# Kernel optimization log

Measured on AMD Instinct MI355X. Metric: run time of the kernel, lower is better.

The kernel has to match this reference:

```python
import jax, jax.numpy as jnp
import numpy as np

D_H = 2048      # d_hidden
D_E = 1408      # d_expert (per routed expert)
E = 8           # n_routed_experts
K = 2           # n_experts_per_token (top-k)
N_SHARED = 2    # n_shared_experts -> shared expert dim = D_E * N_SHARED
B, S = 1, 2048
D_S = D_E * N_SHARED


def setup_inputs() -> dict:
    key = jax.random.key(0)
    ks = jax.random.split(key, 8)
    def init(k, shape, fan_in):
        # nn.Linear default init: U(-1/sqrt(fan_in), 1/sqrt(fan_in))
        bound = 1.0 / np.sqrt(fan_in)
        return jax.random.uniform(k, shape, jnp.float32, -bound, bound)
    x = jax.random.normal(ks[0], (B, S, D_H), jnp.float32)
    gate_W = init(ks[1], (E, D_H), D_H)          # router: logits = x @ gate_W.T
    Wg_e = init(ks[2], (E, D_E, D_H), D_H)       # per-expert W_gate (out,in)
    Wu_e = init(ks[3], (E, D_E, D_H), D_H)       # per-expert W_up
    Wd_e = init(ks[4], (E, D_H, D_E), D_E)       # per-expert W_down
    Wg_s = init(ks[5], (D_S, D_H), D_H)          # shared expert W_gate
    Wu_s = init(ks[6], (D_S, D_H), D_H)
    Wd_s = init(ks[7], (D_H, D_S), D_S)
    return {"x": x, "gate_W": gate_W, "Wg_e": Wg_e, "Wu_e": Wu_e,
            "Wd_e": Wd_e, "Wg_s": Wg_s, "Wu_s": Wu_s, "Wd_s": Wd_s}


def reference(x, gate_W, Wg_e, Wu_e, Wd_e, Wg_s, Wu_s, Wd_s):
    silu = jax.nn.silu
    # shared expert: SiLU-gated MLP over all tokens
    shared = (silu(x @ Wg_s.T) * (x @ Wu_s.T)) @ Wd_s.T          # [B,S,D_H]
    # gating: softmax over experts, then top-k scores/indices
    scores = jax.nn.softmax(x @ gate_W.T, axis=-1)                # [B,S,E]
    topk_scores, topk_idx = jax.lax.top_k(scores, K)              # [B,S,K]
    # dense combine weights w[t,e] = topk score if e selected else 0
    # (equivalent to the torch argsort-dispatch + scatter_reduce sum combine)
    w = jnp.sum(jax.nn.one_hot(topk_idx, E, dtype=x.dtype) * topk_scores[..., None], axis=-2)  # [B,S,E]
    xf = x.reshape(-1, D_H)                                       # [T,D_H], T = B*S
    wf = w.reshape(-1, E)                                         # [T,E]
    # per-expert SiLU-gated MLP, batched over experts
    g = jnp.einsum('td,efd->etf', xf, Wg_e)                       # [E,T,D_E]
    u = jnp.einsum('td,efd->etf', xf, Wu_e)
    h = silu(g) * u
    oe = jnp.einsum('etf,edf->etd', h, Wd_e)                      # [E,T,D_H]
    routed = jnp.einsum('etd,te->td', oe, wf).reshape(B, S, D_H)
    return routed + shared
```

## Files before the change

### kernel.cpp

```cpp
#include <hip/hip_runtime.h>

using short8 = __attribute__((ext_vector_type(8))) short;
using f32x4  = __attribute__((ext_vector_type(4))) float;
typedef unsigned short ushort_t;
typedef unsigned int u32;

#define T_TOK 2048
#define DH 2048
#define DE 1408
#define DS 2816
#define GU_NB 440
#define DN_NB 256

#define NGEc 23068672UL
#define NGSc 5767168UL
#define NXc  4194304UL
#define PA_CVT_BLOCKS 30208
#define PB_CVT_BLOCKS 7040

#define FENCE() asm volatile("" ::: "memory")

__device__ __forceinline__ unsigned short f2bf(float f) {
  unsigned u = __float_as_uint(f);
  u += 0x7FFF + ((u >> 16) & 1);
  return (unsigned short)(u >> 16);
}

__device__ __forceinline__ void gl_lds16(const void* g, void* l) {
  __builtin_amdgcn_global_load_lds((const __attribute__((address_space(1))) u32*)g,
                                   (__attribute__((address_space(3))) u32*)l, 16, 0, 0);
}

__device__ __forceinline__ short8 pack_bf8(float4 a, float4 b) {
  short8 o;
  o[0] = (short)f2bf(a.x); o[1] = (short)f2bf(a.y);
  o[2] = (short)f2bf(a.z); o[3] = (short)f2bf(a.w);
  o[4] = (short)f2bf(b.x); o[5] = (short)f2bf(b.y);
  o[6] = (short)f2bf(b.z); o[7] = (short)f2bf(b.w);
  return o;
}

__global__ void phaseA_kernel(const float* __restrict__ x, const float* __restrict__ gW,
                              int* __restrict__ counts, int* __restrict__ tok_e,
                              int* __restrict__ tok_slot, float* __restrict__ tok_w,
                              const float* __restrict__ Wg_e, const float* __restrict__ Wu_e,
                              const float* __restrict__ Wg_s, const float* __restrict__ Wu_s,
                              ushort_t* wbg_e, ushort_t* wbu_e,
                              ushort_t* wbg_s, ushort_t* wbu_s, ushort_t* xb) {
  int b = blockIdx.x;
  int tid = threadIdx.x;
  if (b < 512) {
    int wid = tid >> 6, lane = tid & 63;
    int t = b * 4 + wid;
    float acc[8] = {0.f,0.f,0.f,0.f,0.f,0.f,0.f,0.f};
    const float* xt = x + (size_t)t * DH;
    for (int i = lane; i < DH; i += 64) {
      float xv = xt[i];
#pragma unroll
      for (int e = 0; e < 8; e++) acc[e] += xv * gW[e * DH + i];
    }
#pragma unroll
    for (int e = 0; e < 8; e++) {
#pragma unroll
      for (int off = 32; off > 0; off >>= 1) acc[e] += __shfl_xor(acc[e], off);
    }
    if (lane == 0) {
      float mx = acc[0];
      for (int e = 1; e < 8; e++) mx = fmaxf(mx, acc[e]);
      float p[8], se = 0.f;
      for (int e = 0; e < 8; e++) { p[e] = __expf(acc[e] - mx); se += p[e]; }
      for (int e = 0; e < 8; e++) p[e] /= se;
      int i1 = 0;
      for (int e = 1; e < 8; e++) if (p[e] > p[i1]) i1 = e;
      int i2 = (i1 == 0) ? 1 : 0;
      for (int e = 0; e < 8; e++) if (e != i1 && p[e] > p[i2]) i2 = e;
      int s1 = atomicAdd(&counts[i1], 1);
      int s2 = atomicAdd(&counts[i2], 1);
      tok_e[2 * t] = i1;     tok_e[2 * t + 1] = i2;
      tok_slot[2 * t] = s1;  tok_slot[2 * t + 1] = s2;
      tok_w[2 * t] = p[i1];  tok_w[2 * t + 1] = p[i2];
    }
    return;
  }
  size_t i = (size_t)(b - 512) * 2048 + (size_t)tid * 8;
  const float* s; ushort_t* d; size_t o;
  if      (i < NGEc)                    { s = Wg_e; d = wbg_e; o = i; }
  else if (i < 2 * NGEc)                { s = Wu_e; d = wbu_e; o = i - NGEc; }
  else if (i < 2 * NGEc + NGSc)         { s = Wg_s; d = wbg_s; o = i - 2 * NGEc; }
  else if (i < 2 * NGEc + 2 * NGSc)     { s = Wu_s; d = wbu_s; o = i - 2 * NGEc - NGSc; }
  else                                  { s = x;    d = xb;    o = i - 2 * NGEc - 2 * NGSc; }
  float4 a = *(const float4*)(s + o);
  float4 bb = *(const float4*)(s + o + 4);
  *(short8*)(d + o) = pack_bf8(a, bb);
}

__global__ void prefix_assign_kernel(const int* __restrict__ counts, int* __restrict__ ebase,
                                     int* __restrict__ gu_off, int* __restrict__ dn_off,
                                     const int* __restrict__ tok_e, int* __restrict__ tok_slot,
                                     int* __restrict__ slot2tok) {
  __shared__ int sbase[8];
  if (threadIdx.x == 0) {
    int a = 0;
    for (int e = 0; e < 8; e++) { sbase[e] = a; ebase[e] = a; a += counts[e]; }
    int g = 0, d = 0;
    for (int z = 0; z < 8; z++) {
      gu_off[z] = g; dn_off[z] = d;
      int Lg = (counts[z] + 255) >> 8;
      g += Lg * 11;
      int Ld = (counts[z] + 255) >> 8;
      d += Ld * 8;
    }
    gu_off[8] = g; g += 88;
    gu_off[9] = g; g += 88;
    gu_off[10] = g;
    dn_off[8] = d; d += 64;
    dn_off[9] = d;
  }
  __syncthreads();
  for (int idx = threadIdx.x; idx < T_TOK * 2; idx += blockDim.x) {
    int e = tok_e[idx];
    int g = sbase[e] + tok_slot[idx];
    tok_slot[idx] = g;
    slot2tok[g] = idx >> 1;
  }
}

__global__ __launch_bounds__(512, 1) void phaseB_kernel(
    const ushort_t* __restrict__ xb, const int* __restrict__ counts,
    const int* __restrict__ ebase, const int* __restrict__ gu_off,
    const int* __restrict__ slot2tok,
    const ushort_t* __restrict__ Wbg_e, const ushort_t* __restrict__ Wbu_e,
    const ushort_t* __restrict__ Wbg_s, const ushort_t* __restrict__ Wbu_s,
    ushort_t* __restrict__ h_r, ushort_t* __restrict__ h_s,
    const float* __restrict__ Wd_e, const float* __restrict__ Wd_s,
    ushort_t* wbd_e, ushort_t* wbd_s) {
  extern __shared__ char smem[];
  int tid = threadIdx.x;
  if (blockIdx.x >= GU_NB) {
    size_t i = (size_t)(blockIdx.x - GU_NB) * 4096 + (size_t)tid * 8;
    const float* s; ushort_t* d; size_t o;
    if (i < NGEc) { s = Wd_e; d = wbd_e; o = i; }
    else          { s = Wd_s; d = wbd_s; o = i - NGEc; }
    float4 a = *(const float4*)(s + o);
    float4 bb = *(const float4*)(s + o + 4);
    *(short8*)(d + o) = pack_bf8(a, bb);
    return;
  }
  int b = blockIdx.x;
  int c = (b & 7) * (GU_NB >> 3) + (b >> 3);
  int off[11];
#pragma unroll
  for (int zz = 0; zz < 11; zz++) off[zz] = gu_off[zz];
  if (c >= off[10]) return;
  int z = 0;
#pragma unroll
  for (int zz = 1; zz < 10; zz++) if (c >= off[zz]) z = zz;
  int cz = c - off[z];

  bool routed = (z < 8);
  int cnt, gbase, Lm;
  const ushort_t *Bg, *Bu;
  if (routed) {
    cnt = counts[z]; gbase = ebase[z];
    Lm = (cnt + 255) >> 8;
    Bg = Wbg_e + (size_t)z * DE * DH;
    Bu = Wbu_e + (size_t)z * DE * DH;
  } else {
    cnt = T_TOK; gbase = 0; Lm = 8;
    Bg = Wbg_s + (size_t)(z - 8) * 1408 * DH;
    Bu = Wbu_s + (size_t)(z - 8) * 1408 * DH;
  }
  int mt = cz % Lm, y = cz / Lm;
  int m0 = mt * 256, n0 = y * 128;

  int lane = tid & 63, w = tid >> 6;
  int lr = lane & 15, lk = lane >> 4;
  int wm = w >> 1, wn = w & 1;

  const ushort_t* asrc[4];
  int adst[4];
#pragma unroll
  for (int j = 0; j < 4; j++) {
    int r = (w * 4 + j) * 8 + (lane >> 3);
    int lrow = m0 + r;
    int tok = routed ? ((lrow < cnt) ? slot2tok[gbase + lrow] : 0) : lrow;
    int cs = (lane & 7) ^ (r & 7);
    asrc[j] = xb + (size_t)tok * DH + cs * 8;
    adst[j] = (w * 4 + j) * 1024;
  }
  const ushort_t* gsrc[2];
  const ushort_t* usrc[2];
  int wdst[2];
#pragma unroll
  for (int j = 0; j < 2; j++) {
    int r = (w * 2 + j) * 8 + (lane >> 3);
    int cs = (lane & 7) ^ (r & 7);
    gsrc[j] = Bg + (size_t)(n0 + r) * DH + cs * 8;
    usrc[j] = Bu + (size_t)(n0 + r) * DH + cs * 8;
    wdst[j] = (w * 2 + j) * 1024;
  }

  f32x4 accg[4][4] = {};
  f32x4 accu[4][4] = {};

#define GU_STAGE(buf, k0)                                             \
  {                                                                   \
    char* ab = smem + (buf) * 32768;                                  \
    char* gb = smem + 65536 + (buf) * 16384;                          \
    char* ub = smem + 98304 + (buf) * 16384;                          \
    _Pragma("unroll")                                                 \
    for (int j = 0; j < 4; j++) gl_lds16(asrc[j] + (k0), ab + adst[j]); \
    _Pragma("unroll")                                                 \
    for (int j = 0; j < 2; j++) {                                     \
      gl_lds16(gsrc[j] + (k0), gb + wdst[j]);                         \
      gl_lds16(usrc[j] + (k0), ub + wdst[j]);                         \
    }                                                                 \
  }

  const int nt = DH >> 6;
  GU_STAGE(0, 0);
  __syncthreads();
  int cur = 0;
  for (int t = 0; t < nt; t++) {
    if (t + 1 < nt) GU_STAGE(cur ^ 1, (t + 1) * 64);
    const char* ab = smem + cur * 32768;
    const char* gb = smem + 65536 + cur * 16384;
    const char* ub = smem + 98304 + cur * 16384;
    short8 af[4][2], bg[4][2], bu[4][2];
#pragma unroll
    for (int m = 0; m < 4; m++) {
#pragma unroll
      for (int ks = 0; ks < 2; ks++) {
        int rr = wm * 64 + m * 16 + lr;
        af[m][ks] = *(const short8*)(ab + rr * 128 + ((ks * 64 + lk * 16) ^ ((rr & 7) << 4)));
      }
    }
#pragma unroll
    for (int n = 0; n < 4; n++) {
#pragma unroll
      for (int ks = 0; ks < 2; ks++) {
        int cc = wn * 64 + n * 16 + lr;
        bg[n][ks] = *(const short8*)(gb + cc * 128 + ((ks * 64 + lk * 16) ^ ((cc & 7) << 4)));
        bu[n][ks] = *(const short8*)(ub + cc * 128 + ((ks * 64 + lk * 16) ^ ((cc & 7) << 4)));
      }
    }
    __builtin_amdgcn_s_setprio(1);
#pragma unroll
    for (int m = 0; m < 4; m++) {
#pragma unroll
      for (int n = 0; n < 4; n++) {
#pragma unroll
        for (int ks = 0; ks < 2; ks++) {
          accg[m][n] = __builtin_amdgcn_mfma_f32_16x16x32_bf16(af[m][ks], bg[n][ks], accg[m][n], 0, 0, 0);
          accu[m][n] = __builtin_amdgcn_mfma_f32_16x16x32_bf16(af[m][ks], bu[n][ks], accu[m][n], 0, 0, 0);
        }
      }
    }
    __builtin_amdgcn_s_setprio(0);
    __syncthreads();
    cur ^= 1;
  }
#pragma unroll
  for (int m = 0; m < 4; m++) {
    int rowl = m0 + wm * 64 + m * 16 + lk * 4;
#pragma unroll
    for (int n = 0; n < 4; n++) {
      int col = n0 + wn * 64 + n * 16 + lr;
#pragma unroll
      for (int j = 0; j < 4; j++) {
        float g = accg[m][n][j], u = accu[m][n][j];
        float s = g / (1.f + __expf(-g));
        unsigned short hv = f2bf(s * u);
        if (routed) {
          if (rowl + j < cnt) h_r[(size_t)(gbase + rowl + j) * DE + col] = hv;
        } else {
          h_s[(size_t)(rowl + j) * DS + (z - 8) * 1408 + col] = hv;
        }
      }
    }
  }
}

__global__ __launch_bounds__(512, 1) void down_kernel(
    const ushort_t* __restrict__ h_r, const ushort_t* __restrict__ h_s,
    const int* __restrict__ counts, const int* __restrict__ ebase,
    const int* __restrict__ dn_off,
    const ushort_t* __restrict__ Wbd_e, const ushort_t* __restrict__ Wbd_s,
    float* __restrict__ oe, float* __restrict__ out) {
  extern __shared__ char smem[];

  int b = blockIdx.x;
  int c = (b & 7) * (DN_NB >> 3) + (b >> 3);
  int off[10];
#pragma unroll
  for (int zz = 0; zz < 10; zz++) off[zz] = dn_off[zz];
  if (c >= off[9]) return;
  int z = 0;
#pragma unroll
  for (int zz = 1; zz < 9; zz++) if (c >= off[zz]) z = zz;
  int cz = c - off[z];

  bool routed = (z < 8);
  int cnt, gbase, K, Lm;
  const ushort_t* Abase;
  const ushort_t* Bw;
  if (routed) {
    cnt = counts[z]; gbase = ebase[z];
    Lm = (cnt + 255) >> 8;
    K = DE;
    Abase = h_r + (size_t)gbase * DE;
    Bw = Wbd_e + (size_t)z * DH * DE;
  } else {
    cnt = T_TOK; gbase = 0; Lm = 8;
    K = DS;
    Abase = h_s;
    Bw = Wbd_s;
  }
  int mt = cz % Lm, y = cz / Lm;
  int m0 = mt * 256, n0 = y * 256;

  int tid = threadIdx.x;
  int lane = tid & 63, w = tid >> 6;
  int lr = lane & 15, lk = lane >> 4;
  int wm = w >> 2, wn = w & 3;

  const ushort_t* asrc[2][2];
  const ushort_t* bsrc[2][2];
  int sdst[2][2];
#pragma unroll
  for (int h = 0; h < 2; h++) {
#pragma unroll
    for (int j = 0; j < 2; j++) {
      int r = h * 128 + (w * 2 + j) * 8 + (lane >> 3);
      int cs = (lane & 7) ^ (r & 7);
      asrc[h][j] = Abase + (size_t)(m0 + r) * K + cs * 8;
      bsrc[h][j] = Bw + (size_t)(n0 + r) * K + cs * 8;
      sdst[h][j] = h * 16384 + (w * 2 + j) * 1024;
    }
  }

  f32x4 acc[8][4] = {};

#define DN_ST_A(p, h, k0)                                              \
  { char* _d = smem + (p) * 32768;                                     \
    gl_lds16(asrc[h][0] + (k0), _d + sdst[h][0]);                      \
    gl_lds16(asrc[h][1] + (k0), _d + sdst[h][1]); }
#define DN_ST_B(p, h, k0)                                              \
  { char* _d = smem + 65536 + (p) * 32768;                             \
    gl_lds16(bsrc[h][0] + (k0), _d + sdst[h][0]);                      \
    gl_lds16(bsrc[h][1] + (k0), _d + sdst[h][1]); }

  const int nt = K >> 6;
  DN_ST_A(0, 0, 0); DN_ST_A(0, 1, 0);
  DN_ST_B(0, 0, 0); DN_ST_B(0, 1, 0);
  DN_ST_B(1, 0, 64); DN_ST_B(1, 1, 64);
  asm volatile("s_waitcnt vmcnt(4)" ::: "memory");
  FENCE(); __builtin_amdgcn_s_barrier(); FENCE();

  short8 bfr[4][2];
  for (int t = 0; t < nt; t++) {
    int p = t & 1;
    const char* ab = smem + p * 32768;
    const char* bb = smem + 65536 + p * 32768;
    int k1 = (t + 1) * 64, k2 = (t + 2) * 64;
#pragma unroll
    for (int ph = 0; ph < 4; ph++) {
      if (ph == 0) {
#pragma unroll
        for (int n = 0; n < 4; n++) {
#pragma unroll
          for (int ks = 0; ks < 2; ks++) {
            int cc = wn * 64 + n * 16 + lr;
            bfr[n][ks] = *(const short8*)(bb + cc * 128 + ((ks * 64 + lk * 16) ^ ((cc & 7) << 4)));
          }
        }
      }
      short8 af[2][2];
#pragma unroll
      for (int m2 = 0; m2 < 2; m2++) {
#pragma unroll
        for (int ks = 0; ks < 2; ks++) {
          int rr = wm * 128 + ph * 32 + m2 * 16 + lr;
          af[m2][ks] = *(const short8*)(ab + rr * 128 + ((ks * 64 + lk * 16) ^ ((rr & 7) << 4)));
        }
      }
      if      (ph == 0) { if (t + 1 < nt) DN_ST_A(p ^ 1, 0, k1); }
      else if (ph == 1) { if (t + 1 < nt) DN_ST_A(p ^ 1, 1, k1); }
      else if (ph == 2) { if (t + 2 < nt) DN_ST_B(p, 0, k2); }
      else {
        if (t + 2 < nt) { DN_ST_B(p, 1, k2); asm volatile("s_waitcnt vmcnt(4)" ::: "memory"); }
        else            {                    asm volatile("s_waitcnt vmcnt(0)" ::: "memory"); }
      }
      FENCE(); __builtin_amdgcn_s_barrier(); FENCE();
      __builtin_amdgcn_s_setprio(1);
#pragma unroll
      for (int m2 = 0; m2 < 2; m2++) {
#pragma unroll
        for (int n = 0; n < 4; n++) {
#pragma unroll
          for (int ks = 0; ks < 2; ks++) {
            acc[ph * 2 + m2][n] = __builtin_amdgcn_mfma_f32_16x16x32_bf16(
                af[m2][ks], bfr[n][ks], acc[ph * 2 + m2][n], 0, 0, 0);
          }
        }
      }
      __builtin_amdgcn_s_setprio(0);
      FENCE(); __builtin_amdgcn_s_barrier(); FENCE();
    }
  }
#pragma unroll
  for (int m = 0; m < 8; m++) {
    int rowl = m0 + wm * 128 + m * 16 + lk * 4;
#pragma unroll
    for (int n = 0; n < 4; n++) {
      int col = n0 + wn * 64 + n * 16 + lr;
#pragma unroll
      for (int j = 0; j < 4; j++) {
        if (routed) {
          if (rowl + j < cnt) oe[(size_t)(gbase + rowl + j) * DH + col] = acc[m][n][j];
        } else {
          out[(size_t)(rowl + j) * DH + col] = acc[m][n][j];
        }
      }
    }
  }
}

__global__ void combine_kernel(const int* __restrict__ tok_gslot,
                               const float* __restrict__ tok_w,
                               const float* __restrict__ oe,
                               float* __restrict__ out) {
  int t = blockIdx.x;
  int g1 = tok_gslot[2 * t], g2 = tok_gslot[2 * t + 1];
  float w1 = tok_w[2 * t], w2 = tok_w[2 * t + 1];
  int i = threadIdx.x * 8;
  const float4* p1 = (const float4*)(oe + (size_t)g1 * DH + i);
  const float4* p2 = (const float4*)(oe + (size_t)g2 * DH + i);
  float4* po = (float4*)(out + (size_t)t * DH + i);
  float4 a0 = p1[0], a1 = p1[1];
  float4 b0 = p2[0], b1 = p2[1];
  float4 o0 = po[0], o1 = po[1];
  o0.x += w1 * a0.x + w2 * b0.x;  o0.y += w1 * a0.y + w2 * b0.y;
  o0.z += w1 * a0.z + w2 * b0.z;  o0.w += w1 * a0.w + w2 * b0.w;
  o1.x += w1 * a1.x + w2 * b1.x;  o1.y += w1 * a1.y + w2 * b1.y;
  o1.z += w1 * a1.z + w2 * b1.z;  o1.w += w1 * a1.w + w2 * b1.w;
  po[0] = o0; po[1] = o1;
}

extern "C" void kernel_launch(void* const* d_in, const int* in_sizes, int n_in,
                              void* d_out, int out_size, void* d_ws, size_t ws_size,
                              hipStream_t stream) {
  const float* x    = (const float*)d_in[0];
  const float* gW   = (const float*)d_in[1];
  const float* Wg_e = (const float*)d_in[2];
  const float* Wu_e = (const float*)d_in[3];
  const float* Wd_e = (const float*)d_in[4];
  const float* Wg_s = (const float*)d_in[5];
  const float* Wu_s = (const float*)d_in[6];
  const float* Wd_s = (const float*)d_in[7];
  float* out = (float*)d_out;

  char* ws = (char*)d_ws;
  int*   counts   = (int*)ws;
  int*   ebase    = (int*)(ws + 64);
  int*   gu_off   = (int*)(ws + 128);
  int*   dn_off   = (int*)(ws + 192);
  int*   tok_e    = (int*)(ws + 256);
  int*   tok_slot = (int*)(ws + 256 + 16384);
  float* tok_w    = (float*)(ws + 256 + 32768);
  int*   slot2tok = (int*)(ws + 256 + 49152);
  ushort_t* xb  = (ushort_t*)(ws + 131072);
  ushort_t* h_r = (ushort_t*)(ws + 131072 + (size_t)T_TOK * DH * 2);
  ushort_t* h_s = h_r + (size_t)4096 * DE;
  float*    oe  = (float*)((char*)h_s + (size_t)T_TOK * DS * 2);
  ushort_t* wb  = (ushort_t*)((char*)oe + (size_t)4096 * DH * 4);
  ushort_t* wbg_e = wb;
  ushort_t* wbu_e = wb + NGEc;
  ushort_t* wbd_e = wb + 2 * NGEc;
  ushort_t* wbg_s = wb + 3 * NGEc;
  ushort_t* wbu_s = wbg_s + NGSc;
  ushort_t* wbd_s = wbg_s + 2 * NGSc;

  hipFuncSetAttribute((const void*)phaseB_kernel,
                      hipFuncAttributeMaxDynamicSharedMemorySize, 131072);
  hipFuncSetAttribute((const void*)down_kernel,
                      hipFuncAttributeMaxDynamicSharedMemorySize, 131072);

  hipMemsetAsync(counts, 0, 64, stream);
  phaseA_kernel<<<512 + PA_CVT_BLOCKS, 256, 0, stream>>>(
      x, gW, counts, tok_e, tok_slot, tok_w,
      Wg_e, Wu_e, Wg_s, Wu_s, wbg_e, wbu_e, wbg_s, wbu_s, xb);
  prefix_assign_kernel<<<1, 256, 0, stream>>>(counts, ebase, gu_off, dn_off,
                                              tok_e, tok_slot, slot2tok);
  phaseB_kernel<<<GU_NB + PB_CVT_BLOCKS, 512, 131072, stream>>>(
      xb, counts, ebase, gu_off, slot2tok, wbg_e, wbu_e, wbg_s, wbu_s, h_r, h_s,
      Wd_e, Wd_s, wbd_e, wbd_s);
  down_kernel<<<DN_NB, 512, 131072, stream>>>(
      h_r, h_s, counts, ebase, dn_off, wbd_e, wbd_s, oe, out);
  combine_kernel<<<T_TOK, 256, 0, stream>>>(tok_slot, tok_w, oe, out);
}
```

Baseline: 338.9 us.

## Store routed expert outputs as bf16 and widen conversion blocks in phase A

```diff
diff --git a/kernel.cpp b/kernel.cpp
--- a/kernel.cpp
+++ b/kernel.cpp
@@ -15,7 +15,7 @@
 #define NGEc 23068672UL
 #define NGSc 5767168UL
 #define NXc  4194304UL
-#define PA_CVT_BLOCKS 30208
+#define PA_CVT_BLOCKS 7552
 #define PB_CVT_BLOCKS 7040
 
 #define FENCE() asm volatile("" ::: "memory")
@@ -24,6 +24,10 @@
   unsigned u = __float_as_uint(f);
   u += 0x7FFF + ((u >> 16) & 1);
   return (unsigned short)(u >> 16);
+}
+
+__device__ __forceinline__ float bf2f(short v) {
+  return __uint_as_float(((u32)(unsigned short)v) << 16);
 }
 
 __device__ __forceinline__ void gl_lds16(const void* g, void* l) {
@@ -49,9 +53,9 @@
                               ushort_t* wbg_s, ushort_t* wbu_s, ushort_t* xb) {
   int b = blockIdx.x;
   int tid = threadIdx.x;
-  if (b < 512) {
+  if (b < 256) {
     int wid = tid >> 6, lane = tid & 63;
-    int t = b * 4 + wid;
+    int t = b * 8 + wid;
     float acc[8] = {0.f,0.f,0.f,0.f,0.f,0.f,0.f,0.f};
     const float* xt = x + (size_t)t * DH;
     for (int i = lane; i < DH; i += 64) {
@@ -82,16 +86,19 @@
     }
     return;
   }
-  size_t i = (size_t)(b - 512) * 2048 + (size_t)tid * 8;
+  size_t i = (size_t)(b - 256) * 8192 + (size_t)tid * 16;
   const float* s; ushort_t* d; size_t o;
   if      (i < NGEc)                    { s = Wg_e; d = wbg_e; o = i; }
   else if (i < 2 * NGEc)                { s = Wu_e; d = wbu_e; o = i - NGEc; }
   else if (i < 2 * NGEc + NGSc)         { s = Wg_s; d = wbg_s; o = i - 2 * NGEc; }
   else if (i < 2 * NGEc + 2 * NGSc)     { s = Wu_s; d = wbu_s; o = i - 2 * NGEc - NGSc; }
   else                                  { s = x;    d = xb;    o = i - 2 * NGEc - 2 * NGSc; }
-  float4 a = *(const float4*)(s + o);
-  float4 bb = *(const float4*)(s + o + 4);
-  *(short8*)(d + o) = pack_bf8(a, bb);
+  float4 a0 = *(const float4*)(s + o);
+  float4 b0 = *(const float4*)(s + o + 4);
+  float4 a1 = *(const float4*)(s + o + 8);
+  float4 b1 = *(const float4*)(s + o + 12);
+  *(short8*)(d + o)     = pack_bf8(a0, b0);
+  *(short8*)(d + o + 8) = pack_bf8(a1, b1);
 }
 
 __global__ void prefix_assign_kernel(const int* __restrict__ counts, int* __restrict__ ebase,
@@ -286,7 +293,7 @@
     const int* __restrict__ counts, const int* __restrict__ ebase,
     const int* __restrict__ dn_off,
     const ushort_t* __restrict__ Wbd_e, const ushort_t* __restrict__ Wbd_s,
-    float* __restrict__ oe, float* __restrict__ out) {
+    ushort_t* __restrict__ oe, float* __restrict__ out) {
   extern __shared__ char smem[];
 
   int b = blockIdx.x;
@@ -417,7 +424,8 @@
 #pragma unroll
       for (int j = 0; j < 4; j++) {
         if (routed) {
-          if (rowl + j < cnt) oe[(size_t)(gbase + rowl + j) * DH + col] = acc[m][n][j];
+          if (rowl + j < cnt)
+            oe[(size_t)(gbase + rowl + j) * DH + col] = f2bf(acc[m][n][j]);
         } else {
           out[(size_t)(rowl + j) * DH + col] = acc[m][n][j];
         }
@@ -428,22 +436,24 @@
 
 __global__ void combine_kernel(const int* __restrict__ tok_gslot,
                                const float* __restrict__ tok_w,
-                               const float* __restrict__ oe,
+                               const ushort_t* __restrict__ oe,
                                float* __restrict__ out) {
   int t = blockIdx.x;
   int g1 = tok_gslot[2 * t], g2 = tok_gslot[2 * t + 1];
   float w1 = tok_w[2 * t], w2 = tok_w[2 * t + 1];
   int i = threadIdx.x * 8;
-  const float4* p1 = (const float4*)(oe + (size_t)g1 * DH + i);
-  const float4* p2 = (const float4*)(oe + (size_t)g2 * DH + i);
+  short8 a = *(const short8*)(oe + (size_t)g1 * DH + i);
+  short8 b = *(const short8*)(oe + (size_t)g2 * DH + i);
   float4* po = (float4*)(out + (size_t)t * DH + i);
-  float4 a0 = p1[0], a1 = p1[1];
-  float4 b0 = p2[0], b1 = p2[1];
   float4 o0 = po[0], o1 = po[1];
-  o0.x += w1 * a0.x + w2 * b0.x;  o0.y += w1 * a0.y + w2 * b0.y;
-  o0.z += w1 * a0.z + w2 * b0.z;  o0.w += w1 * a0.w + w2 * b0.w;
-  o1.x += w1 * a1.x + w2 * b1.x;  o1.y += w1 * a1.y + w2 * b1.y;
-  o1.z += w1 * a1.z + w2 * b1.z;  o1.w += w1 * a1.w + w2 * b1.w;
+  o0.x += w1 * bf2f(a[0]) + w2 * bf2f(b[0]);
+  o0.y += w1 * bf2f(a[1]) + w2 * bf2f(b[1]);
+  o0.z += w1 * bf2f(a[2]) + w2 * bf2f(b[2]);
+  o0.w += w1 * bf2f(a[3]) + w2 * bf2f(b[3]);
+  o1.x += w1 * bf2f(a[4]) + w2 * bf2f(b[4]);
+  o1.y += w1 * bf2f(a[5]) + w2 * bf2f(b[5]);
+  o1.z += w1 * bf2f(a[6]) + w2 * bf2f(b[6]);
+  o1.w += w1 * bf2f(a[7]) + w2 * bf2f(b[7]);
   po[0] = o0; po[1] = o1;
 }
 
@@ -472,7 +482,7 @@
   ushort_t* xb  = (ushort_t*)(ws + 131072);
   ushort_t* h_r = (ushort_t*)(ws + 131072 + (size_t)T_TOK * DH * 2);
   ushort_t* h_s = h_r + (size_t)4096 * DE;
-  float*    oe  = (float*)((char*)h_s + (size_t)T_TOK * DS * 2);
+  ushort_t* oe  = (ushort_t*)((char*)h_s + (size_t)T_TOK * DS * 2);
   ushort_t* wb  = (ushort_t*)((char*)oe + (size_t)4096 * DH * 4);
   ushort_t* wbg_e = wb;
   ushort_t* wbu_e = wb + NGEc;
@@ -487,7 +497,7 @@
                       hipFuncAttributeMaxDynamicSharedMemorySize, 131072);
 
   hipMemsetAsync(counts, 0, 64, stream);
-  phaseA_kernel<<<512 + PA_CVT_BLOCKS, 256, 0, stream>>>(
+  phaseA_kernel<<<256 + PA_CVT_BLOCKS, 512, 0, stream>>>(
       x, gW, counts, tok_e, tok_slot, tok_w,
       Wg_e, Wu_e, Wg_s, Wu_s, wbg_e, wbu_e, wbg_s, wbu_s, xb);
   prefix_assign_kernel<<<1, 256, 0, stream>>>(counts, ebase, gu_off, dn_off,
```

Result: no change. 336.1 us (median of 2 runs) (-0.8%).
